# Kernel optimization log

Hardware: AMD Instinct MI355X
Metric: run time of the kernel (lower is better)

## Reference

```python
import jax, jax.numpy as jnp
import numpy as np

D_MODEL = 1024
N_HEADS = 16
D_K = D_MODEL // N_HEADS
B, S = 2, 2048


def setup_inputs() -> dict:
    key = jax.random.key(0)
    ks = jax.random.split(key, 12)
    sc = 1.0 / np.sqrt(D_MODEL)
    inp = {
        "Q": jax.random.normal(ks[0], (B, S, D_MODEL), jnp.float32),
        "K": jax.random.normal(ks[1], (B, S, D_MODEL), jnp.float32),
        "V": jax.random.normal(ks[2], (B, S, D_MODEL), jnp.float32),
        # causal mask: 0 where disallowed (masked_fill(mask==0, -inf))
        "mask": jnp.broadcast_to(jnp.tril(jnp.ones((S, S), jnp.int32))[None, None], (B, 1, S, S)),
        "Wq": jax.random.normal(ks[3], (D_MODEL, D_MODEL), jnp.float32) * sc,
        "bq": jnp.zeros((D_MODEL,), jnp.float32),
        "Wk": jax.random.normal(ks[4], (D_MODEL, D_MODEL), jnp.float32) * sc,
        "bk": jnp.zeros((D_MODEL,), jnp.float32),
        "Wv": jax.random.normal(ks[5], (D_MODEL, D_MODEL), jnp.float32) * sc,
        "bv": jnp.zeros((D_MODEL,), jnp.float32),
        "Wo": jax.random.normal(ks[6], (D_MODEL, D_MODEL), jnp.float32) * sc,
        "bo": jnp.zeros((D_MODEL,), jnp.float32),
    }
    return inp


def reference(Q, K, V, mask, Wq, bq, Wk, bk, Wv, bv, Wo, bo):
    b = Q.shape[0]
    # projections, split heads: [b, h, s, d_k]
    def proj(x, W, bias):
        y = x @ W.T + bias
        return y.reshape(b, -1, N_HEADS, D_K).transpose(0, 2, 1, 3)
    q = proj(Q, Wq, bq)
    k = proj(K, Wk, bk)
    v = proj(V, Wv, bv)
    scores = jnp.einsum('bhsd,bhtd->bhst', q, k) / jnp.sqrt(jnp.float32(D_K))
    scores = jnp.where(mask == 0, jnp.finfo(scores.dtype).min, scores)
    attn = jax.nn.softmax(scores, axis=-1)  # [b, h, s, s]
    out = jnp.einsum('bhst,bhtd->bhsd', attn, v)
    out = out.transpose(0, 2, 1, 3).reshape(b, -1, D_MODEL)
    out = out @ Wo.T + bo  # dropout is identity in eval mode
    return out, attn
```

## Files before the change

kernel.cpp:

```cpp
#include <hip/hip_runtime.h>
#include <math.h>

#define D_MODEL 1024
#define NH 16
#define DK 64
#define BB 2
#define SS 2048
#define BH (BB * NH)
#define M_TOT (BB * SS)
#define QBLK 128
#define NSTRIP (SS / QBLK)

typedef __bf16 bf16x8 __attribute__((ext_vector_type(8)));
typedef float f32x4 __attribute__((ext_vector_type(4)));

static __device__ __forceinline__ unsigned short f2bf(float x) {
  unsigned int u = __float_as_uint(x);
  u = (u + 0x7fffu + ((u >> 16) & 1u)) >> 16;
  return (unsigned short)u;
}

__global__ __launch_bounds__(256) void cvt_all_82592221102086(
    const float* __restrict__ Q, const float* __restrict__ K,
    const float* __restrict__ V, const float* __restrict__ Wq,
    const float* __restrict__ Wk, const float* __restrict__ Wv,
    const float* __restrict__ Wo, unsigned short* __restrict__ Qc,
    unsigned short* __restrict__ Kc, unsigned short* __restrict__ Vc,
    unsigned short* __restrict__ Wqc, unsigned short* __restrict__ Wkc,
    unsigned short* __restrict__ Wvc, unsigned short* __restrict__ Woc) {
  const int id = blockIdx.x;
  const float* s;
  unsigned short* d;
  int c0;
  if (id < 2048) { s = Q; d = Qc; c0 = id * 256; }
  else if (id < 4096) { s = K; d = Kc; c0 = (id - 2048) * 256; }
  else if (id < 6144) { s = V; d = Vc; c0 = (id - 4096) * 256; }
  else {
    const int w = (id - 6144) >> 9, off = (id - 6144) & 511;
    s = (w == 0) ? Wq : (w == 1) ? Wk : (w == 2) ? Wv : Wo;
    d = (w == 0) ? Wqc : (w == 1) ? Wkc : (w == 2) ? Wvc : Woc;
    c0 = off * 256;
  }
  const size_t i = (size_t)c0 + threadIdx.x;
  const float4* sp = reinterpret_cast<const float4*>(s) + 2 * i;
  float4 a = sp[0], b = sp[1];
  union { unsigned short us[8]; uint4 u4; } pk;
  pk.us[0] = f2bf(a.x); pk.us[1] = f2bf(a.y);
  pk.us[2] = f2bf(a.z); pk.us[3] = f2bf(a.w);
  pk.us[4] = f2bf(b.x); pk.us[5] = f2bf(b.y);
  pk.us[6] = f2bf(b.z); pk.us[7] = f2bf(b.w);
  *(reinterpret_cast<uint4*>(d) + i) = pk.u4;
}

template <int MODE>
static __device__ __forceinline__ void proj_body(
    const unsigned short* __restrict__ X, const unsigned short* __restrict__ W,
    const float* __restrict__ bias, void* __restrict__ Yv, int m0, int n0) {
  __shared__ __align__(16) unsigned short As[128][72];
  __shared__ __align__(16) unsigned short Bs[64][72];
  const int tid = threadIdx.x;
  const int wave = tid >> 6, lane = tid & 63;
  const int lrow = lane & 15, lkc = lane >> 4;

  f32x4 acc[2][4] = {};

  for (int kt = 0; kt < D_MODEL; kt += 64) {
    __syncthreads();
#pragma unroll
    for (int i = 0; i < 4; ++i) {
      int c = tid + 256 * i, r = c >> 3, c8 = (c & 7) * 8;
      *reinterpret_cast<uint4*>(&As[r][c8]) = *reinterpret_cast<const uint4*>(
          &X[(size_t)(m0 + r) * D_MODEL + kt + c8]);
    }
#pragma unroll
    for (int i = 0; i < 2; ++i) {
      int c = tid + 256 * i, r = c >> 3, c8 = (c & 7) * 8;
      *reinterpret_cast<uint4*>(&Bs[r][c8]) = *reinterpret_cast<const uint4*>(
          &W[(size_t)(n0 + r) * D_MODEL + kt + c8]);
    }
    __syncthreads();
#pragma unroll
    for (int kk = 0; kk < 64; kk += 32) {
      bf16x8 a0 = *reinterpret_cast<const bf16x8*>(
          &As[wave * 32 + lrow][kk + lkc * 8]);
      bf16x8 a1 = *reinterpret_cast<const bf16x8*>(
          &As[wave * 32 + 16 + lrow][kk + lkc * 8]);
#pragma unroll
      for (int nj = 0; nj < 4; ++nj) {
        bf16x8 b = *reinterpret_cast<const bf16x8*>(
            &Bs[nj * 16 + lrow][kk + lkc * 8]);
        acc[0][nj] = __builtin_amdgcn_mfma_f32_16x16x32_bf16(a0, b, acc[0][nj], 0, 0, 0);
        acc[1][nj] = __builtin_amdgcn_mfma_f32_16x16x32_bf16(a1, b, acc[1][nj], 0, 0, 0);
      }
    }
  }

  const int h = n0 >> 6;
#pragma unroll
  for (int mi = 0; mi < 2; ++mi) {
#pragma unroll
    for (int nj = 0; nj < 4; ++nj) {
      const int d = nj * 16 + lrow;
      const float bv = bias[n0 + d];
#pragma unroll
      for (int j = 0; j < 4; ++j) {
        const int m = m0 + wave * 32 + mi * 16 + lkc * 4 + j;
        const float val = acc[mi][nj][j] + bv;
        if (MODE == 0) {
          const int b = m >> 11, s = m & 2047;
          reinterpret_cast<unsigned short*>(Yv)
              [((size_t)(b * NH + h) * SS + s) * DK + d] = f2bf(val);
        } else {
          reinterpret_cast<float*>(Yv)[(size_t)m * D_MODEL + n0 + d] = val;
        }
      }
    }
  }
}

__global__ __launch_bounds__(256) void proj_qkv_82592221102086(
    const unsigned short* __restrict__ Qc, const unsigned short* __restrict__ Kc,
    const unsigned short* __restrict__ Vc, const unsigned short* __restrict__ Wqc,
    const unsigned short* __restrict__ Wkc, const unsigned short* __restrict__ Wvc,
    const float* __restrict__ bq, const float* __restrict__ bk,
    const float* __restrict__ bv, unsigned short* __restrict__ qbv,
    unsigned short* __restrict__ kbv, unsigned short* __restrict__ vbv) {
  const unsigned short *X, *W;
  const float* bias;
  unsigned short* Y;
  if (blockIdx.z == 0) { X = Qc; W = Wqc; bias = bq; Y = qbv; }
  else if (blockIdx.z == 1) { X = Kc; W = Wkc; bias = bk; Y = kbv; }
  else { X = Vc; W = Wvc; bias = bv; Y = vbv; }
  proj_body<0>(X, W, bias, Y, blockIdx.y * 128, blockIdx.x * 64);
}

__global__ __launch_bounds__(256) void proj_out_82592221102086(
    const unsigned short* __restrict__ X, const unsigned short* __restrict__ W,
    const float* __restrict__ bias, float* __restrict__ Y) {
  proj_body<1>(X, W, bias, Y, blockIdx.y * 128, blockIdx.x * 64);
}

__global__ __launch_bounds__(512, 4) void attn_mfma_82592221102086(
    const unsigned short* __restrict__ qb, const unsigned short* __restrict__ kb,
    const unsigned short* __restrict__ vb, float* __restrict__ attn,
    unsigned short* __restrict__ ctx) {
  __shared__ __align__(16) unsigned short Ks[64][72];
  __shared__ __align__(16) unsigned short Vt[64][72];
  __shared__ __align__(16) unsigned short Ps[QBLK][76];
  __shared__ __align__(16) float Pf[QBLK][76];

  const int bi = blockIdx.x;
  const int xcd = bi & 7, slot = bi >> 3;
  const int bhl = (slot >> 4) & 3;
  const int bh = xcd * 4 + bhl;
  const int u = slot & 15;
  const int qt = (bhl & 2) ? (15 - u) : u;
  const int qs = qt * QBLK;
  const int ntile = 2 * qt + 2;
  const int tid = threadIdx.x;
  const int wave = tid >> 6, lane = tid & 63;
  const int lrow = lane & 15, lkc = lane >> 4;

  const unsigned short* qrow =
      qb + ((size_t)bh * SS + qs + wave * 16 + lrow) * DK;
  const bf16x8 qf0 = *reinterpret_cast<const bf16x8*>(qrow + lkc * 8);
  const bf16x8 qf1 = *reinterpret_cast<const bf16x8*>(qrow + 32 + lkc * 8);

  float lsum[4] = {};

  for (int kt = 0; kt < ntile; ++kt) {
    const int ks = kt * 64;
    __syncthreads();
    {
      const int r = tid >> 3, c8 = (tid & 7) * 8;
      *reinterpret_cast<uint4*>(&Ks[r][c8]) = *reinterpret_cast<const uint4*>(
          &kb[((size_t)bh * SS + ks + r) * DK + c8]);
    }
    __syncthreads();

    f32x4 sacc[4] = {};
#pragma unroll
    for (int kk = 0; kk < 64; kk += 32) {
      const bf16x8 qf = (kk == 0) ? qf0 : qf1;
#pragma unroll
      for (int tj = 0; tj < 4; ++tj) {
        bf16x8 kf = *reinterpret_cast<const bf16x8*>(
            &Ks[tj * 16 + lrow][kk + lkc * 8]);
        sacc[tj] = __builtin_amdgcn_mfma_f32_16x16x32_bf16(qf, kf, sacc[tj], 0, 0, 0);
      }
    }
    const bool diag = (kt >= ntile - 2);
#pragma unroll
    for (int tj = 0; tj < 4; ++tj) {
#pragma unroll
      for (int j = 0; j < 4; ++j) {
        const int grow = qs + wave * 16 + lkc * 4 + j;
        const int gcol = ks + tj * 16 + lrow;
        if (!diag || gcol <= grow)
          lsum[j] += __expf(fminf(sacc[tj][j] * 0.125f, 80.f));
      }
    }
  }

  float inv[4];
#pragma unroll
  for (int j = 0; j < 4; ++j) {
    float l = lsum[j];
#pragma unroll
    for (int m = 1; m < 16; m <<= 1) l += __shfl_xor(l, m, 64);
    inv[j] = 1.0f / l;
  }

  f32x4 oacc[4] = {};

  for (int kt = 0; kt < ntile; ++kt) {
    const int ks = kt * 64;
    __syncthreads();
    {
      const int r = tid >> 3, c8 = (tid & 7) * 8;
      *reinterpret_cast<uint4*>(&Ks[r][c8]) = *reinterpret_cast<const uint4*>(
          &kb[((size_t)bh * SS + ks + r) * DK + c8]);
    }
    {
      const int t = tid >> 3, d0 = (tid & 7) * 8;
      uint4 raw = *reinterpret_cast<const uint4*>(
          &vb[((size_t)bh * SS + ks + t) * DK + d0]);
      const unsigned short* pv = reinterpret_cast<const unsigned short*>(&raw);
      const int tsw = t ^ d0;
#pragma unroll
      for (int jj = 0; jj < 8; ++jj) Vt[d0 + jj][tsw] = pv[jj];
    }
    __syncthreads();

    f32x4 sacc[4] = {};
#pragma unroll
    for (int kk = 0; kk < 64; kk += 32) {
      const bf16x8 qf = (kk == 0) ? qf0 : qf1;
#pragma unroll
      for (int tj = 0; tj < 4; ++tj) {
        bf16x8 kf = *reinterpret_cast<const bf16x8*>(
            &Ks[tj * 16 + lrow][kk + lkc * 8]);
        sacc[tj] = __builtin_amdgcn_mfma_f32_16x16x32_bf16(qf, kf, sacc[tj], 0, 0, 0);
      }
    }

    const bool diag = (kt >= ntile - 2);
#pragma unroll
    for (int tj = 0; tj < 4; ++tj) {
#pragma unroll
      for (int j = 0; j < 4; ++j) {
        const int prow = wave * 16 + lkc * 4 + j;
        const int grow = qs + prow;
        const int gcol = ks + tj * 16 + lrow;
        float pv = 0.f;
        if (!diag || gcol <= grow)
          pv = __expf(fminf(sacc[tj][j] * 0.125f, 80.f)) * inv[j];
        Pf[prow][tj * 16 + lrow] = pv;
        Ps[prow][tj * 16 + lrow] = f2bf(pv);
      }
    }
    __syncthreads();

#pragma unroll
    for (int it = 0; it < 4; ++it) {
      const int r = it * 32 + (tid >> 4), c0 = (tid & 15) * 4;
      const f32x4 v = *reinterpret_cast<const f32x4*>(&Pf[r][c0]);
      __builtin_nontemporal_store(
          v, reinterpret_cast<f32x4*>(
                 &attn[((size_t)bh * SS + qs + r) * SS + ks + c0]));
    }

#pragma unroll
    for (int kk2 = 0; kk2 < 64; kk2 += 32) {
      bf16x8 pf = *reinterpret_cast<const bf16x8*>(
          &Ps[wave * 16 + lrow][kk2 + lkc * 8]);
#pragma unroll
      for (int dj = 0; dj < 4; ++dj) {
        const int d = dj * 16 + lrow;
        const int tch = ((kk2 >> 3) + lkc) ^ (d >> 3);
        bf16x8 vf = *reinterpret_cast<const bf16x8*>(&Vt[d][tch << 3]);
        oacc[dj] = __builtin_amdgcn_mfma_f32_16x16x32_bf16(pf, vf, oacc[dj], 0, 0, 0);
      }
    }
  }

  const int b = bh >> 4, h = bh & 15;
#pragma unroll
  for (int dj = 0; dj < 4; ++dj) {
    const int d = dj * 16 + lrow;
#pragma unroll
    for (int j = 0; j < 4; ++j) {
      const int row = qs + wave * 16 + lkc * 4 + j;
      ctx[((size_t)(b * SS + row)) * D_MODEL + h * DK + d] = f2bf(oacc[dj][j]);
    }
  }

  const f32x4 z4 = {0.f, 0.f, 0.f, 0.f};
  for (int kt = ntile; kt < 32; ++kt) {
    const int ks = kt * 64;
#pragma unroll
    for (int it = 0; it < 4; ++it) {
      const int r = it * 32 + (tid >> 4), c0 = (tid & 15) * 4;
      __builtin_nontemporal_store(
          z4, reinterpret_cast<f32x4*>(
                  &attn[((size_t)bh * SS + qs + r) * SS + ks + c0]));
    }
  }
}

extern "C" void kernel_launch(void* const* d_in, const int* in_sizes, int n_in,
                              void* d_out, int out_size, void* d_ws,
                              size_t ws_size, hipStream_t stream) {
  const float* Q = (const float*)d_in[0];
  const float* K = (const float*)d_in[1];
  const float* V = (const float*)d_in[2];
  const float* Wq = (const float*)d_in[4];
  const float* bq = (const float*)d_in[5];
  const float* Wk = (const float*)d_in[6];
  const float* bk = (const float*)d_in[7];
  const float* Wv = (const float*)d_in[8];
  const float* bv = (const float*)d_in[9];
  const float* Wo = (const float*)d_in[10];
  const float* bo = (const float*)d_in[11];

  float* out = (float*)d_out;
  float* attn = out + (size_t)M_TOT * D_MODEL;

  const size_t nX = (size_t)M_TOT * D_MODEL;
  const size_t nW = (size_t)D_MODEL * D_MODEL;
  unsigned short* ws = (unsigned short*)d_ws;
  unsigned short* Qc = ws;
  unsigned short* Kc = Qc + nX;
  unsigned short* Vc = Kc + nX;
  unsigned short* Wqc = Vc + nX;
  unsigned short* Wkc = Wqc + nW;
  unsigned short* Wvc = Wkc + nW;
  unsigned short* Woc = Wvc + nW;
  unsigned short* qbv = Woc + nW;
  unsigned short* kbv = qbv + nX;
  unsigned short* vbv = kbv + nX;
  unsigned short* ctx = vbv + nX;

  cvt_all_82592221102086<<<8192, 256, 0, stream>>>(
      Q, K, V, Wq, Wk, Wv, Wo, Qc, Kc, Vc, Wqc, Wkc, Wvc, Woc);

  proj_qkv_82592221102086<<<dim3(D_MODEL / 64, M_TOT / 128, 3), 256, 0,
                            stream>>>(Qc, Kc, Vc, Wqc, Wkc, Wvc, bq, bk, bv,
                                      qbv, kbv, vbv);

  attn_mfma_82592221102086<<<dim3(BH * NSTRIP), 512, 0, stream>>>(
      qbv, kbv, vbv, attn, ctx);

  proj_out_82592221102086<<<dim3(D_MODEL / 64, M_TOT / 128), 256, 0, stream>>>(
      ctx, Woc, bo, out);
}
```

Measured before the change: 789.5 us.

## Fuse fp32-to-bf16 conversion into projection GEMMs, widen tiles, store attn directly

Removes the separate conversion kernel and its bf16 workspace copies; the projection GEMMs now load fp32 inputs and weights and convert them while filling shared memory. The N tile grows from 64 to 128, so each block holds twice as many accumulators and the grid has half as many blocks. In the attention kernel the fp32 staging buffer and its barrier are gone, and each thread writes probabilities straight to the attn output with scalar nontemporal stores. The scalar writes are less coalesced than the earlier 16-byte row stores, which risks slowing the attn write that dominates memory traffic.

```diff
diff --git a/kernel.cpp b/kernel.cpp
--- a/kernel.cpp
+++ b/kernel.cpp
@@ -20,63 +20,45 @@
   return (unsigned short)u;
 }
 
-__global__ __launch_bounds__(256) void cvt_all_82592221102086(
-    const float* __restrict__ Q, const float* __restrict__ K,
-    const float* __restrict__ V, const float* __restrict__ Wq,
-    const float* __restrict__ Wk, const float* __restrict__ Wv,
-    const float* __restrict__ Wo, unsigned short* __restrict__ Qc,
-    unsigned short* __restrict__ Kc, unsigned short* __restrict__ Vc,
-    unsigned short* __restrict__ Wqc, unsigned short* __restrict__ Wkc,
-    unsigned short* __restrict__ Wvc, unsigned short* __restrict__ Woc) {
-  const int id = blockIdx.x;
-  const float* s;
-  unsigned short* d;
-  int c0;
-  if (id < 2048) { s = Q; d = Qc; c0 = id * 256; }
-  else if (id < 4096) { s = K; d = Kc; c0 = (id - 2048) * 256; }
-  else if (id < 6144) { s = V; d = Vc; c0 = (id - 4096) * 256; }
-  else {
-    const int w = (id - 6144) >> 9, off = (id - 6144) & 511;
-    s = (w == 0) ? Wq : (w == 1) ? Wk : (w == 2) ? Wv : Wo;
-    d = (w == 0) ? Wqc : (w == 1) ? Wkc : (w == 2) ? Wvc : Woc;
-    c0 = off * 256;
-  }
-  const size_t i = (size_t)c0 + threadIdx.x;
-  const float4* sp = reinterpret_cast<const float4*>(s) + 2 * i;
-  float4 a = sp[0], b = sp[1];
-  union { unsigned short us[8]; uint4 u4; } pk;
-  pk.us[0] = f2bf(a.x); pk.us[1] = f2bf(a.y);
-  pk.us[2] = f2bf(a.z); pk.us[3] = f2bf(a.w);
-  pk.us[4] = f2bf(b.x); pk.us[5] = f2bf(b.y);
-  pk.us[6] = f2bf(b.z); pk.us[7] = f2bf(b.w);
-  *(reinterpret_cast<uint4*>(d) + i) = pk.u4;
-}
-
-template <int MODE>
+static __device__ __forceinline__ bf16x8 cvt8(float4 a, float4 b) {
+  bf16x8 v;
+  v[0] = (__bf16)a.x; v[1] = (__bf16)a.y; v[2] = (__bf16)a.z; v[3] = (__bf16)a.w;
+  v[4] = (__bf16)b.x; v[5] = (__bf16)b.y; v[6] = (__bf16)b.z; v[7] = (__bf16)b.w;
+  return v;
+}
+
+template <int IN_F32, int MODE>
 static __device__ __forceinline__ void proj_body(
-    const unsigned short* __restrict__ X, const unsigned short* __restrict__ W,
+    const void* __restrict__ Xv, const float* __restrict__ W,
     const float* __restrict__ bias, void* __restrict__ Yv, int m0, int n0) {
   __shared__ __align__(16) unsigned short As[128][72];
-  __shared__ __align__(16) unsigned short Bs[64][72];
+  __shared__ __align__(16) unsigned short Bs[128][72];
   const int tid = threadIdx.x;
   const int wave = tid >> 6, lane = tid & 63;
   const int lrow = lane & 15, lkc = lane >> 4;
 
-  f32x4 acc[2][4] = {};
+  f32x4 acc[2][8] = {};
 
   for (int kt = 0; kt < D_MODEL; kt += 64) {
     __syncthreads();
 #pragma unroll
     for (int i = 0; i < 4; ++i) {
-      int c = tid + 256 * i, r = c >> 3, c8 = (c & 7) * 8;
-      *reinterpret_cast<uint4*>(&As[r][c8]) = *reinterpret_cast<const uint4*>(
-          &X[(size_t)(m0 + r) * D_MODEL + kt + c8]);
-    }
-#pragma unroll
-    for (int i = 0; i < 2; ++i) {
-      int c = tid + 256 * i, r = c >> 3, c8 = (c & 7) * 8;
-      *reinterpret_cast<uint4*>(&Bs[r][c8]) = *reinterpret_cast<const uint4*>(
-          &W[(size_t)(n0 + r) * D_MODEL + kt + c8]);
+      const int u = tid + 256 * i, r = u >> 3, c8 = (u & 7) * 8;
+      if (IN_F32) {
+        const float4* xp = reinterpret_cast<const float4*>(
+            (const float*)Xv + (size_t)(m0 + r) * D_MODEL + kt + c8);
+        *reinterpret_cast<bf16x8*>(&As[r][c8]) = cvt8(xp[0], xp[1]);
+      } else {
+        *reinterpret_cast<uint4*>(&As[r][c8]) = *reinterpret_cast<const uint4*>(
+            (const unsigned short*)Xv + (size_t)(m0 + r) * D_MODEL + kt + c8);
+      }
+    }
+#pragma unroll
+    for (int i = 0; i < 4; ++i) {
+      const int u = tid + 256 * i, r = u >> 3, c8 = (u & 7) * 8;
+      const float4* wp = reinterpret_cast<const float4*>(
+          W + (size_t)(n0 + r) * D_MODEL + kt + c8);
+      *reinterpret_cast<bf16x8*>(&Bs[r][c8]) = cvt8(wp[0], wp[1]);
     }
     __syncthreads();
 #pragma unroll
@@ -86,7 +68,7 @@
       bf16x8 a1 = *reinterpret_cast<const bf16x8*>(
           &As[wave * 32 + 16 + lrow][kk + lkc * 8]);
 #pragma unroll
-      for (int nj = 0; nj < 4; ++nj) {
+      for (int nj = 0; nj < 8; ++nj) {
         bf16x8 b = *reinterpret_cast<const bf16x8*>(
             &Bs[nj * 16 + lrow][kk + lkc * 8]);
         acc[0][nj] = __builtin_amdgcn_mfma_f32_16x16x32_bf16(a0, b, acc[0][nj], 0, 0, 0);
@@ -95,23 +77,23 @@
     }
   }
 
-  const int h = n0 >> 6;
 #pragma unroll
   for (int mi = 0; mi < 2; ++mi) {
 #pragma unroll
-    for (int nj = 0; nj < 4; ++nj) {
-      const int d = nj * 16 + lrow;
-      const float bv = bias[n0 + d];
+    for (int nj = 0; nj < 8; ++nj) {
+      const int nfull = n0 + nj * 16 + lrow;
+      const float bv = bias[nfull];
 #pragma unroll
       for (int j = 0; j < 4; ++j) {
         const int m = m0 + wave * 32 + mi * 16 + lkc * 4 + j;
         const float val = acc[mi][nj][j] + bv;
         if (MODE == 0) {
           const int b = m >> 11, s = m & 2047;
+          const int h = nfull >> 6, d = nfull & 63;
           reinterpret_cast<unsigned short*>(Yv)
               [((size_t)(b * NH + h) * SS + s) * DK + d] = f2bf(val);
         } else {
-          reinterpret_cast<float*>(Yv)[(size_t)m * D_MODEL + n0 + d] = val;
+          reinterpret_cast<float*>(Yv)[(size_t)m * D_MODEL + nfull] = val;
         }
       }
     }
@@ -119,25 +101,24 @@
 }
 
 __global__ __launch_bounds__(256) void proj_qkv_82592221102086(
-    const unsigned short* __restrict__ Qc, const unsigned short* __restrict__ Kc,
-    const unsigned short* __restrict__ Vc, const unsigned short* __restrict__ Wqc,
-    const unsigned short* __restrict__ Wkc, const unsigned short* __restrict__ Wvc,
+    const float* __restrict__ Q, const float* __restrict__ K,
+    const float* __restrict__ V, const float* __restrict__ Wq,
+    const float* __restrict__ Wk, const float* __restrict__ Wv,
     const float* __restrict__ bq, const float* __restrict__ bk,
     const float* __restrict__ bv, unsigned short* __restrict__ qbv,
     unsigned short* __restrict__ kbv, unsigned short* __restrict__ vbv) {
-  const unsigned short *X, *W;
-  const float* bias;
+  const float *X, *W, *bias;
   unsigned short* Y;
-  if (blockIdx.z == 0) { X = Qc; W = Wqc; bias = bq; Y = qbv; }
-  else if (blockIdx.z == 1) { X = Kc; W = Wkc; bias = bk; Y = kbv; }
-  else { X = Vc; W = Wvc; bias = bv; Y = vbv; }
-  proj_body<0>(X, W, bias, Y, blockIdx.y * 128, blockIdx.x * 64);
+  if (blockIdx.z == 0) { X = Q; W = Wq; bias = bq; Y = qbv; }
+  else if (blockIdx.z == 1) { X = K; W = Wk; bias = bk; Y = kbv; }
+  else { X = V; W = Wv; bias = bv; Y = vbv; }
+  proj_body<1, 0>(X, W, bias, Y, blockIdx.y * 128, blockIdx.x * 128);
 }
 
 __global__ __launch_bounds__(256) void proj_out_82592221102086(
-    const unsigned short* __restrict__ X, const unsigned short* __restrict__ W,
-    const float* __restrict__ bias, float* __restrict__ Y) {
-  proj_body<1>(X, W, bias, Y, blockIdx.y * 128, blockIdx.x * 64);
+    const unsigned short* __restrict__ ctx, const float* __restrict__ Wo,
+    const float* __restrict__ bo, float* __restrict__ out) {
+  proj_body<0, 1>(ctx, Wo, bo, out, blockIdx.y * 128, blockIdx.x * 128);
 }
 
 __global__ __launch_bounds__(512, 4) void attn_mfma_82592221102086(
@@ -147,7 +128,6 @@
   __shared__ __align__(16) unsigned short Ks[64][72];
   __shared__ __align__(16) unsigned short Vt[64][72];
   __shared__ __align__(16) unsigned short Ps[QBLK][76];
-  __shared__ __align__(16) float Pf[QBLK][76];
 
   const int bi = blockIdx.x;
   const int xcd = bi & 7, slot = bi >> 3;
@@ -255,21 +235,11 @@
         float pv = 0.f;
         if (!diag || gcol <= grow)
           pv = __expf(fminf(sacc[tj][j] * 0.125f, 80.f)) * inv[j];
-        Pf[prow][tj * 16 + lrow] = pv;
-        Ps[prow][tj * 16 + lrow] = f2bf(pv);
-      }
-    }
-    __syncthreads();
-
-#pragma unroll
-    for (int it = 0; it < 4; ++it) {
-      const int r = it * 32 + (tid >> 4), c0 = (tid & 15) * 4;
-      const f32x4 v = *reinterpret_cast<const f32x4*>(&Pf[r][c0]);
-      __builtin_nontemporal_store(
-          v, reinterpret_cast<f32x4*>(
-                 &attn[((size_t)bh * SS + qs + r) * SS + ks + c0]));
-    }
-
+        __builtin_nontemporal_store(
+            pv, &attn[((size_t)bh * SS + grow) * SS + gcol]);
+        *reinterpret_cast<__bf16*>(&Ps[prow][tj * 16 + lrow]) = (__bf16)pv;
+      }
+    }
 #pragma unroll
     for (int kk2 = 0; kk2 < 64; kk2 += 32) {
       bf16x8 pf = *reinterpret_cast<const bf16x8*>(
@@ -327,30 +297,19 @@
   float* attn = out + (size_t)M_TOT * D_MODEL;
 
   const size_t nX = (size_t)M_TOT * D_MODEL;
-  const size_t nW = (size_t)D_MODEL * D_MODEL;
   unsigned short* ws = (unsigned short*)d_ws;
-  unsigned short* Qc = ws;
-  unsigned short* Kc = Qc + nX;
-  unsigned short* Vc = Kc + nX;
-  unsigned short* Wqc = Vc + nX;
-  unsigned short* Wkc = Wqc + nW;
-  unsigned short* Wvc = Wkc + nW;
-  unsigned short* Woc = Wvc + nW;
-  unsigned short* qbv = Woc + nW;
+  unsigned short* qbv = ws;
   unsigned short* kbv = qbv + nX;
   unsigned short* vbv = kbv + nX;
   unsigned short* ctx = vbv + nX;
 
-  cvt_all_82592221102086<<<8192, 256, 0, stream>>>(
-      Q, K, V, Wq, Wk, Wv, Wo, Qc, Kc, Vc, Wqc, Wkc, Wvc, Woc);
-
-  proj_qkv_82592221102086<<<dim3(D_MODEL / 64, M_TOT / 128, 3), 256, 0,
-                            stream>>>(Qc, Kc, Vc, Wqc, Wkc, Wvc, bq, bk, bv,
+  proj_qkv_82592221102086<<<dim3(D_MODEL / 128, M_TOT / 128, 3), 256, 0,
+                            stream>>>(Q, K, V, Wq, Wk, Wv, bq, bk, bv,
                                       qbv, kbv, vbv);
 
   attn_mfma_82592221102086<<<dim3(BH * NSTRIP), 512, 0, stream>>>(
       qbv, kbv, vbv, attn, ctx);
 
-  proj_out_82592221102086<<<dim3(D_MODEL / 64, M_TOT / 128), 256, 0, stream>>>(
-      ctx, Woc, bo, out);
-}
+  proj_out_82592221102086<<<dim3(D_MODEL / 128, M_TOT / 128), 256, 0, stream>>>(
+      ctx, Wo, bo, out);
+}
```

After: 815.9 us. 1.03x slower.
